# Kernel optimization log

Measured on AMD Instinct MI355X. Metric: run time of the kernel, lower is better.

## Reference

```python
import jax, jax.numpy as jnp
import numpy as np
import math

H = 8        # num_heads
D = 32       # dim_head
DEPTH = 1
LAMBDA_INIT = 0.8 - 0.6 * math.exp(-0.3 * DEPTH)
EPS = 1e-8


def setup_inputs() -> dict:
    key = jax.random.key(0)
    ks = jax.random.split(key, 9)
    B, T, IN_DIM, OUT_DIM = 2, 2048, 1024, 1024
    E = 2 * H * D  # 512
    inp = {
        "x": jax.random.normal(ks[0], (B, T, IN_DIM), dtype=jnp.float32),
        "Wq": jax.random.normal(ks[1], (IN_DIM, E), dtype=jnp.float32) * (IN_DIM ** -0.5),
        "Wkv": jax.random.normal(ks[2], (IN_DIM, 2 * E), dtype=jnp.float32) * (IN_DIM ** -0.5),
        "Wout": jax.random.normal(ks[3], (E, OUT_DIM), dtype=jnp.float32) * (E ** -0.5),
        "lambda_q1": 0.1 * jax.random.normal(ks[4], (D,), dtype=jnp.float32),
        "lambda_k1": 0.1 * jax.random.normal(ks[5], (D,), dtype=jnp.float32),
        "lambda_q2": 0.1 * jax.random.normal(ks[6], (D,), dtype=jnp.float32),
        "lambda_k2": 0.1 * jax.random.normal(ks[7], (D,), dtype=jnp.float32),
        "gamma": jnp.ones((2 * D,), dtype=jnp.float32),
    }
    return inp


def reference(x, Wq, Wkv, Wout, lambda_q1, lambda_k1, lambda_q2, lambda_k2, gamma):
    B, T, _ = x.shape
    scaling = D ** -0.5

    q = (x @ Wq).reshape(B, T, 2 * H, D).transpose(0, 2, 1, 3) * scaling  # [B,2H,T,D]
    kv = x @ Wkv
    k, v = jnp.split(kv, 2, axis=-1)
    k = k.reshape(B, T, 2 * H, D).transpose(0, 2, 1, 3)        # [B,2H,T,D]
    v = v.reshape(B, T, H, 2 * D).transpose(0, 2, 1, 3)        # [B,H,T,2D]

    dots = jnp.einsum('bhqd,bhkd->bhqk', q, k)                 # [B,2H,T,T]
    attn_w = jax.nn.softmax(dots.astype(jnp.float32), axis=-1).astype(dots.dtype)

    lam1 = jnp.exp(jnp.sum(lambda_q1 * lambda_k1))
    lam2 = jnp.exp(jnp.sum(lambda_q2 * lambda_k2))
    lam = lam1 - lam2 + LAMBDA_INIT

    attn_w = attn_w.reshape(B, H, 2, T, T)
    attn_w = attn_w[:, :, 0] - lam * attn_w[:, :, 1]           # [B,H,T,T]

    attn = jnp.einsum('bhqk,bhkd->bhqd', attn_w, v)            # [B,H,T,2D]

    rms = jnp.sqrt(jnp.mean(attn * attn, axis=-1, keepdims=True))
    attn = gamma * (attn / (rms + EPS))
    attn = attn * (1.0 - LAMBDA_INIT)

    attn = attn.transpose(0, 2, 1, 3).reshape(B, T, 2 * H * D)  # [B,T,E]
    return attn @ Wout
```

## Files before the change

kernel.cpp:

```cpp
#include <hip/hip_runtime.h>

typedef __attribute__((ext_vector_type(8)))  _Float16 half8;
typedef __attribute__((ext_vector_type(4)))  _Float16 half4;
typedef __attribute__((ext_vector_type(2)))  __fp16   fp16x2;
typedef __attribute__((ext_vector_type(4)))  float    f32x4;

#define MFMA16(a,b,c) __builtin_amdgcn_mfma_f32_16x16x32_f16(a,b,c,0,0,0)

#define QSCALE       0.17677669529663687f
#define LAMBDA_INIT  0.3555090675909693f
#define OUT_SCALE    0.6444909324090307f
#define LOG2E        1.4426950408889634f
#define MSHIFT       4.0f

#define EXP2(x) __builtin_amdgcn_exp2f(x)

__device__ __forceinline__ void gld16(const void* g, void* l) {
    __builtin_amdgcn_global_load_lds(
        (const __attribute__((address_space(1))) unsigned int*)g,
        (__attribute__((address_space(3))) unsigned int*)l, 16, 0, 0);
}

__device__ __forceinline__ void tr64(const float* __restrict__ src,
                                     _Float16* __restrict__ dst,
                                     int srcld, int dstld, int bx, int by) {
    __shared__ float t[64][65];
    int k0 = bx * 64, n0 = by * 64;
    int c = threadIdx.x & 63, rr = threadIdx.x >> 6;
#pragma unroll
    for (int ph = 0; ph < 16; ++ph) {
        int k = ph * 4 + rr;
        t[k][c] = src[(size_t)(k0 + k) * srcld + n0 + c];
    }
    __syncthreads();
#pragma unroll
    for (int ph = 0; ph < 16; ++ph) {
        int n = ph * 4 + rr;
        dst[(size_t)(n0 + n) * dstld + k0 + c] = (_Float16)t[c][n];
    }
}

__global__ __launch_bounds__(256) void k_prep(const float* __restrict__ x,
                                              const float* __restrict__ Wq,
                                              const float* __restrict__ Wkv,
                                              const float* __restrict__ Wout,
                                              _Float16* __restrict__ xh,
                                              _Float16* __restrict__ WallT,
                                              _Float16* __restrict__ WoutT) {
    int b = blockIdx.x;
    if (b < 4096) {
        int i = (b * 256 + threadIdx.x) * 4;
        f32x4 v = *(const f32x4*)(x + i);
        half4 h;
        h[0] = (_Float16)v[0]; h[1] = (_Float16)v[1];
        h[2] = (_Float16)v[2]; h[3] = (_Float16)v[3];
        *(half4*)(xh + i) = h;
    } else if (b < 4224) {
        int idx = b - 4096;
        tr64(Wq, WallT, 512, 1024, idx & 15, idx >> 4);
    } else if (b < 4480) {
        int idx = b - 4224;
        tr64(Wkv, WallT + 512 * 1024, 1024, 1024, idx & 15, idx >> 4);
    } else {
        int idx = b - 4480;
        tr64(Wout, WoutT, 1024, 512, idx & 7, idx >> 3);
    }
}

__device__ __forceinline__ void gemm_loop(const _Float16* __restrict__ A,
                                          const _Float16* __restrict__ Bt,
                                          int K, int bm, int bn,
                                          char* As, char* Bs,
                                          f32x4 (&acc)[4][4]) {
    int tid = threadIdx.x, lane = tid & 63, w = tid >> 6;
    int col16 = lane & 15, quad = lane >> 4;
    int wm = (w >> 1) << 6, wn = (w & 1) << 6;
    int r0 = tid >> 2;
    int kc = (tid & 3) << 3;
    const _Float16* ga0 = A  + (size_t)(bm + r0) * K + kc;
    const _Float16* ga1 = A  + (size_t)(bm + 64 + r0) * K + kc;
    const _Float16* gb0 = Bt + (size_t)(bn + r0) * K + kc;
    const _Float16* gb1 = Bt + (size_t)(bn + 64 + r0) * K + kc;
    char* lA = As + (w << 10);
    char* lB = Bs + (w << 10);

    for (int k0 = 0; k0 < K; k0 += 32) {
        __syncthreads();
        gld16(ga0 + k0, lA);
        gld16(ga1 + k0, lA + 4096);
        gld16(gb0 + k0, lB);
        gld16(gb1 + k0, lB + 4096);
        __syncthreads();
        half8 af[4], bf[4];
#pragma unroll
        for (int i = 0; i < 4; ++i)
            af[i] = *(const half8*)(As + ((wm + i * 16 + col16) << 6) + (quad << 4));
#pragma unroll
        for (int j = 0; j < 4; ++j)
            bf[j] = *(const half8*)(Bs + ((wn + j * 16 + col16) << 6) + (quad << 4));
#pragma unroll
        for (int i = 0; i < 4; ++i)
#pragma unroll
            for (int j = 0; j < 4; ++j)
                acc[i][j] = MFMA16(af[i], bf[j], acc[i][j]);
    }
}

__global__ __launch_bounds__(256) void k_gemm_qkv(const _Float16* __restrict__ xh,
                                                  const _Float16* __restrict__ WallT,
                                                  _Float16* __restrict__ qbuf,
                                                  char* __restrict__ Kf,
                                                  char* __restrict__ Vf) {
    __shared__ __align__(16) char As[8192];
    __shared__ __align__(16) char Bs[8192];
    f32x4 acc[4][4] = {};
    int bm = blockIdx.x * 128, bn = blockIdx.y * 128;
    gemm_loop(xh, WallT, 1024, bm, bn, As, Bs, acc);

    int tid = threadIdx.x, lane = tid & 63, w = tid >> 6;
    int col16 = lane & 15, quad = lane >> 4;
    int wm = (w >> 1) << 6, wn = (w & 1) << 6;

    if (bn < 512) {
        const float s = QSCALE * LOG2E;
#pragma unroll
        for (int i = 0; i < 4; ++i)
#pragma unroll
            for (int j = 0; j < 4; ++j) {
                int n = bn + wn + j * 16 + col16;
                int m0 = bm + wm + i * 16 + quad * 4;
#pragma unroll
                for (int r = 0; r < 4; ++r)
                    qbuf[(size_t)(m0 + r) * 512 + n] = (_Float16)(acc[i][j][r] * s);
            }
    } else if (bn < 1024) {
#pragma unroll
        for (int j = 0; j < 4; ++j) {
            int n = bn + wn + j * 16 + col16 - 512;
            int pp = n >> 6, dd = n & 63, head = dd >> 5, d32 = dd & 31;
            int lbase = (d32 >> 3) << 4;
            int e2 = (d32 & 7) << 1;
            int fragb = head << 11;
#pragma unroll
            for (int i = 0; i < 4; ++i) {
                int m0 = bm + wm + i * 16 + quad * 4;
                int b = m0 >> 11, tok = m0 & 2047, kb = tok >> 5, kk = tok & 31;
                char* dst = Kf + (((size_t)((b * 8 + pp) * 64 + kb)) << 12)
                          + fragb + ((kk >> 4) << 10) + ((lbase + (kk & 15)) << 4) + e2;
#pragma unroll
                for (int r = 0; r < 4; ++r)
                    *(_Float16*)(dst + (r << 4)) = (_Float16)acc[i][j][r];
            }
        }
    } else {
#pragma unroll
        for (int j = 0; j < 4; ++j) {
            int n = bn + wn + j * 16 + col16 - 1024;
            int pp = n >> 6, ch = n & 63;
            int off_t = ((ch >> 4) << 10) + ((ch & 15) << 4);
#pragma unroll
            for (int i = 0; i < 4; ++i) {
                int m0 = bm + wm + i * 16 + quad * 4;
                int b = m0 >> 11, tok = m0 & 2047, kb = tok >> 5, kk = tok & 31;
                int quadv = (kk < 16) ? (kk >> 2) : ((kk - 16) >> 2);
                int e0 = (kk < 16) ? 0 : 4;
                half4 hv;
#pragma unroll
                for (int r = 0; r < 4; ++r) hv[r] = (_Float16)acc[i][j][r];
                *(half4*)(Vf + (((size_t)((b * 8 + pp) * 64 + kb)) << 12)
                          + off_t + (quadv << 8) + (e0 << 1)) = hv;
            }
        }
    }
}

__global__ __launch_bounds__(256) void k_attn(const _Float16* __restrict__ qbuf,
                                              const char* __restrict__ Kf,
                                              const char* __restrict__ Vf,
                                              _Float16* __restrict__ Po0,
                                              _Float16* __restrict__ Po1,
                                              float* __restrict__ Pl,
                                              int nc) {
    __shared__ __align__(16) char Sh[32768];

    int blk = blockIdx.x;
    int qt = blk & 31, p = (blk >> 5) & 7, bb = (blk >> 8) & 1, c = blk >> 9;
    int tid = threadIdx.x, lane = tid & 63, w = tid >> 6;
    int col16 = lane & 15, quad = lane >> 4;
    int iters = 32 / nc;

    int qrow = bb * 2048 + qt * 64 + w * 16 + col16;
    const _Float16* qb = qbuf + (size_t)qrow * 512 + p * 64;
    half8 q1 = *(const half8*)(qb + quad * 8);
    half8 q2 = *(const half8*)(qb + 32 + quad * 8);

    size_t choff = (size_t)c * ((size_t)iters << 13);
    const char* Kb = Kf + (((size_t)(bb * 8 + p)) << 18) + choff;
    const char* Vb = Vf + (((size_t)(bb * 8 + p)) << 18) + choff;
    const f32x4 minit = {-MSHIFT, -MSHIFT, -MSHIFT, -MSHIFT};
    int t16 = tid << 4;

    float l1 = 0.f, l2 = 0.f;
    f32x4 o1[4] = {}, o2[4] = {};
    {
        gld16(Kb + t16, Sh + t16);          gld16(Kb + 4096 + t16, Sh + 4096 + t16);
        gld16(Vb + t16, Sh + 8192 + t16);   gld16(Vb + 4096 + t16, Sh + 12288 + t16);
    }
    for (int it = 0; it < iters; ++it) {
        __syncthreads();
        const char* cur = Sh + ((it & 1) << 14);
        if (it + 1 < iters) {
            const char* sk = Kb + ((size_t)(it + 1) << 13);
            const char* sv = Vb + ((size_t)(it + 1) << 13);
            char* d = Sh + (((it + 1) & 1) << 14);
            gld16(sk + t16, d + t16);          gld16(sk + 4096 + t16, d + 4096 + t16);
            gld16(sv + t16, d + 8192 + t16);   gld16(sv + 4096 + t16, d + 12288 + t16);
        }
#pragma unroll
        for (int g = 0; g < 2; ++g) {
            const char* kbase = cur + (g << 12) + (lane << 4);
            const char* vbase = cur + 8192 + (g << 12) + (lane << 4);
            half8 kf0 = *(const half8*)(kbase);
            half8 kf1 = *(const half8*)(kbase + 1024);
            half8 kf2 = *(const half8*)(kbase + 2048);
            half8 kf3 = *(const half8*)(kbase + 3072);
            f32x4 sa1 = MFMA16(kf0, q1, minit), sb1 = MFMA16(kf1, q1, minit);
            f32x4 sa2 = MFMA16(kf2, q2, minit), sb2 = MFMA16(kf3, q2, minit);

            union { half8 v; fp16x2 h[4]; } p1u, p2u;
            {
                float a0 = EXP2(sa1[0]), a1 = EXP2(sa1[1]);
                float a2 = EXP2(sa1[2]), a3 = EXP2(sa1[3]);
                float b0 = EXP2(sb1[0]), b1 = EXP2(sb1[1]);
                float b2 = EXP2(sb1[2]), b3 = EXP2(sb1[3]);
                l1 += ((a0 + a1) + (a2 + a3)) + ((b0 + b1) + (b2 + b3));
                p1u.h[0] = __builtin_amdgcn_cvt_pkrtz(a0, a1);
                p1u.h[1] = __builtin_amdgcn_cvt_pkrtz(a2, a3);
                p1u.h[2] = __builtin_amdgcn_cvt_pkrtz(b0, b1);
                p1u.h[3] = __builtin_amdgcn_cvt_pkrtz(b2, b3);
            }
            {
                float a0 = EXP2(sa2[0]), a1 = EXP2(sa2[1]);
                float a2 = EXP2(sa2[2]), a3 = EXP2(sa2[3]);
                float b0 = EXP2(sb2[0]), b1 = EXP2(sb2[1]);
                float b2 = EXP2(sb2[2]), b3 = EXP2(sb2[3]);
                l2 += ((a0 + a1) + (a2 + a3)) + ((b0 + b1) + (b2 + b3));
                p2u.h[0] = __builtin_amdgcn_cvt_pkrtz(a0, a1);
                p2u.h[1] = __builtin_amdgcn_cvt_pkrtz(a2, a3);
                p2u.h[2] = __builtin_amdgcn_cvt_pkrtz(b0, b1);
                p2u.h[3] = __builtin_amdgcn_cvt_pkrtz(b2, b3);
            }
            half8 vf0 = *(const half8*)(vbase);
            half8 vf1 = *(const half8*)(vbase + 1024);
            half8 vf2 = *(const half8*)(vbase + 2048);
            half8 vf3 = *(const half8*)(vbase + 3072);
            o1[0] = MFMA16(p1u.v, vf0, o1[0]); o2[0] = MFMA16(p2u.v, vf0, o2[0]);
            o1[1] = MFMA16(p1u.v, vf1, o1[1]); o2[1] = MFMA16(p2u.v, vf1, o2[1]);
            o1[2] = MFMA16(p1u.v, vf2, o1[2]); o2[2] = MFMA16(p2u.v, vf2, o2[2]);
            o1[3] = MFMA16(p1u.v, vf3, o1[3]); o2[3] = MFMA16(p2u.v, vf3, o2[3]);
        }
    }
    l1 += __shfl_xor(l1, 16); l1 += __shfl_xor(l1, 32);
    l2 += __shfl_xor(l2, 16); l2 += __shfl_xor(l2, 32);

    _Float16* Po = (c == 0) ? Po0 : Po1;
    int rowbase = (bb * 8 + p) * 2048 + qt * 64 + w * 16;
    _Float16* PoC = Po + (size_t)rowbase * 128;
#pragma unroll
    for (int r = 0; r < 4; ++r) {
        int rl = quad * 4 + r;
        _Float16* dst = PoC + (size_t)rl * 128 + col16;
#pragma unroll
        for (int t = 0; t < 4; ++t) {
            dst[t * 16]      = (_Float16)o1[t][r];
            dst[64 + t * 16] = (_Float16)o2[t][r];
        }
    }
    if (quad == 0) {
        int idx = rowbase + col16;
        Pl[c * 65536 + idx]         = l1;
        Pl[c * 65536 + 32768 + idx] = l2;
    }
}

__global__ __launch_bounds__(256) void k_combine(const _Float16* __restrict__ Po0,
                                                 const _Float16* __restrict__ Po1,
                                                 const float* __restrict__ Pl,
                                                 const float* __restrict__ lq1,
                                                 const float* __restrict__ lk1,
                                                 const float* __restrict__ lq2,
                                                 const float* __restrict__ lk2,
                                                 const float* __restrict__ gamma,
                                                 _Float16* __restrict__ attnO,
                                                 int nc) {
    int gid = blockIdx.x * 256 + threadIdx.x;
    int idx = gid >> 4, j = gid & 15;

    float s1 = 0.f, s2 = 0.f;
#pragma unroll
    for (int i = 0; i < 32; ++i) { s1 += lq1[i] * lk1[i]; s2 += lq2[i] * lk2[i]; }
    float lam = __expf(s1) - __expf(s2) + LAMBDA_INIT;

    size_t rb = (size_t)idx * 128 + j * 4;
    half4 c1a = *(const half4*)(Po0 + rb);
    half4 c2a = *(const half4*)(Po0 + rb + 64);
    float l1 = Pl[idx], l2 = Pl[32768 + idx];
    float o1[4], o2[4];
#pragma unroll
    for (int e = 0; e < 4; ++e) { o1[e] = (float)c1a[e]; o2[e] = (float)c2a[e]; }
    if (nc == 2) {
        half4 c1b = *(const half4*)(Po1 + rb);
        half4 c2b = *(const half4*)(Po1 + rb + 64);
        l1 += Pl[65536 + idx]; l2 += Pl[65536 + 32768 + idx];
#pragma unroll
        for (int e = 0; e < 4; ++e) { o1[e] += (float)c1b[e]; o2[e] += (float)c2b[e]; }
    }
    float il1 = 1.f / l1, il2 = lam / l2;
    float Of[4], ss = 0.f;
#pragma unroll
    for (int e = 0; e < 4; ++e) {
        Of[e] = o1[e] * il1 - o2[e] * il2;
        ss += Of[e] * Of[e];
    }
    ss += __shfl_xor(ss, 1, 16); ss += __shfl_xor(ss, 2, 16);
    ss += __shfl_xor(ss, 4, 16); ss += __shfl_xor(ss, 8, 16);
    float rms = sqrtf(ss * 0.015625f);
    float sc = OUT_SCALE / (rms + 1e-8f);

    int b = idx >> 14, p = (idx >> 11) & 7, t = idx & 2047;
    half4 o;
#pragma unroll
    for (int e = 0; e < 4; ++e) o[e] = (_Float16)(gamma[j * 4 + e] * Of[e] * sc);
    *(half4*)(attnO + ((size_t)(b * 2048 + t) * 512) + p * 64 + j * 4) = o;
}

__global__ __launch_bounds__(256) void k_gemm_out(const _Float16* __restrict__ attn,
                                                  const _Float16* __restrict__ WoutT,
                                                  float* __restrict__ out) {
    __shared__ __align__(16) char As[8192];
    __shared__ __align__(16) char Bs[8192];
    f32x4 acc[4][4] = {};
    int bm = blockIdx.x * 128, bn = blockIdx.y * 128;
    gemm_loop(attn, WoutT, 512, bm, bn, As, Bs, acc);

    int tid = threadIdx.x, lane = tid & 63, w = tid >> 6;
    int col16 = lane & 15, quad = lane >> 4;
    int wm = (w >> 1) << 6, wn = (w & 1) << 6;
#pragma unroll
    for (int i = 0; i < 4; ++i)
#pragma unroll
        for (int j = 0; j < 4; ++j) {
            int n = bn + wn + j * 16 + col16;
            int m0 = bm + wm + i * 16 + quad * 4;
#pragma unroll
            for (int r = 0; r < 4; ++r)
                out[(size_t)(m0 + r) * 1024 + n] = acc[i][j][r];
        }
}

extern "C" void kernel_launch(void* const* d_in, const int* in_sizes, int n_in,
                              void* d_out, int out_size, void* d_ws, size_t ws_size,
                              hipStream_t stream) {
    const float* x     = (const float*)d_in[0];
    const float* Wq    = (const float*)d_in[1];
    const float* Wkv   = (const float*)d_in[2];
    const float* Wout  = (const float*)d_in[3];
    const float* lq1   = (const float*)d_in[4];
    const float* lk1   = (const float*)d_in[5];
    const float* lq2   = (const float*)d_in[6];
    const float* lk2   = (const float*)d_in[7];
    const float* gamma = (const float*)d_in[8];
    float* out = (float*)d_out;

    char* ws = (char*)d_ws;
    _Float16* xh    = (_Float16*)(ws);
    _Float16* Po0   = (_Float16*)(ws);
    _Float16* WallT = (_Float16*)(ws + 8388608);
    float*    Pl    = (float*)(ws + 8388608);
    _Float16* WoutT = (_Float16*)(ws + 11534336);
    _Float16* qbuf  = (_Float16*)(ws + 12582912);
    char*     Kf    = (char*)(ws + 16777216);
    char*     Vf    = (char*)(ws + 20971520);
    _Float16* attn  = (_Float16*)(ws + 25165824);
    _Float16* Po1   = (_Float16*)(ws + 29360128);

    int nc = (ws_size >= 37748736u) ? 2 : 1;

    k_prep<<<4608, 256, 0, stream>>>(x, Wq, Wkv, Wout, xh, WallT, WoutT);
    k_gemm_qkv<<<dim3(32, 12), 256, 0, stream>>>(xh, WallT, qbuf, Kf, Vf);
    k_attn<<<nc * 512, 256, 0, stream>>>(qbuf, Kf, Vf, Po0, Po1, Pl, nc);
    k_combine<<<2048, 256, 0, stream>>>(Po0, Po1, Pl, lq1, lk1, lq2, lk2, gamma, attn, nc);
    k_gemm_out<<<dim3(32, 8), 256, 0, stream>>>(attn, WoutT, out);
}
```

Before: 169.0 us.

## Fuse attention split-K combine into attention kernel with in-block chunk reduction

Replaces the separate attention and combine kernels with one kernel of 512-thread blocks, where 4 wave pairs each cover a quarter of the key range for 32 query rows. Partial outputs and row sums are reduced through shared memory, and the lambda-difference, RMS norm and output store happen in the same block. This removes the global round trip of fp16 partials and one launch. The new loop drops double buffering and uses two barriers per iteration, so load latency is no longer overlapped with compute.

```diff
diff --git a/kernel.cpp b/kernel.cpp
--- a/kernel.cpp
+++ b/kernel.cpp
@@ -174,164 +174,137 @@
     }
 }
 
-__global__ __launch_bounds__(256) void k_attn(const _Float16* __restrict__ qbuf,
-                                              const char* __restrict__ Kf,
-                                              const char* __restrict__ Vf,
-                                              _Float16* __restrict__ Po0,
-                                              _Float16* __restrict__ Po1,
-                                              float* __restrict__ Pl,
-                                              int nc) {
+__global__ __launch_bounds__(512, 8) void k_attn_fused(
+        const _Float16* __restrict__ qbuf,
+        const char* __restrict__ Kf,
+        const char* __restrict__ Vf,
+        const float* __restrict__ lq1,
+        const float* __restrict__ lk1,
+        const float* __restrict__ lq2,
+        const float* __restrict__ lk2,
+        const float* __restrict__ gamma,
+        _Float16* __restrict__ attnO) {
     __shared__ __align__(16) char Sh[32768];
+    __shared__ float Ls[2][8][16];
 
     int blk = blockIdx.x;
-    int qt = blk & 31, p = (blk >> 5) & 7, bb = (blk >> 8) & 1, c = blk >> 9;
+    int r32 = blk & 63, p = (blk >> 6) & 7, bb = blk >> 9;
     int tid = threadIdx.x, lane = tid & 63, w = tid >> 6;
+    int qt2 = w & 1, c = w >> 1;
     int col16 = lane & 15, quad = lane >> 4;
-    int iters = 32 / nc;
-
-    int qrow = bb * 2048 + qt * 64 + w * 16 + col16;
+
+    int qrow = bb * 2048 + r32 * 32 + qt2 * 16 + col16;
     const _Float16* qb = qbuf + (size_t)qrow * 512 + p * 64;
     half8 q1 = *(const half8*)(qb + quad * 8);
     half8 q2 = *(const half8*)(qb + 32 + quad * 8);
 
-    size_t choff = (size_t)c * ((size_t)iters << 13);
-    const char* Kb = Kf + (((size_t)(bb * 8 + p)) << 18) + choff;
-    const char* Vb = Vf + (((size_t)(bb * 8 + p)) << 18) + choff;
+    size_t bpoff = ((size_t)(bb * 8 + p)) << 18;
+    const char* src2 = ((tid >= 256) ? Vf : Kf) + bpoff + ((tid & 255) << 4);
+    int dbase = ((tid >= 256) ? 4096 : 0) + ((tid & 255) << 4);
+
+    const char* kvb = Sh + (c << 13) + (lane << 4);
     const f32x4 minit = {-MSHIFT, -MSHIFT, -MSHIFT, -MSHIFT};
-    int t16 = tid << 4;
 
     float l1 = 0.f, l2 = 0.f;
     f32x4 o1[4] = {}, o2[4] = {};
-    {
-        gld16(Kb + t16, Sh + t16);          gld16(Kb + 4096 + t16, Sh + 4096 + t16);
-        gld16(Vb + t16, Sh + 8192 + t16);   gld16(Vb + 4096 + t16, Sh + 12288 + t16);
-    }
-    for (int it = 0; it < iters; ++it) {
+
+    for (int it = 0; it < 16; ++it) {
         __syncthreads();
-        const char* cur = Sh + ((it & 1) << 14);
-        if (it + 1 < iters) {
-            const char* sk = Kb + ((size_t)(it + 1) << 13);
-            const char* sv = Vb + ((size_t)(it + 1) << 13);
-            char* d = Sh + (((it + 1) & 1) << 14);
-            gld16(sk + t16, d + t16);          gld16(sk + 4096 + t16, d + 4096 + t16);
-            gld16(sv + t16, d + 8192 + t16);   gld16(sv + 4096 + t16, d + 12288 + t16);
-        }
-#pragma unroll
-        for (int g = 0; g < 2; ++g) {
-            const char* kbase = cur + (g << 12) + (lane << 4);
-            const char* vbase = cur + 8192 + (g << 12) + (lane << 4);
-            half8 kf0 = *(const half8*)(kbase);
-            half8 kf1 = *(const half8*)(kbase + 1024);
-            half8 kf2 = *(const half8*)(kbase + 2048);
-            half8 kf3 = *(const half8*)(kbase + 3072);
-            f32x4 sa1 = MFMA16(kf0, q1, minit), sb1 = MFMA16(kf1, q1, minit);
-            f32x4 sa2 = MFMA16(kf2, q2, minit), sb2 = MFMA16(kf3, q2, minit);
-
-            union { half8 v; fp16x2 h[4]; } p1u, p2u;
-            {
-                float a0 = EXP2(sa1[0]), a1 = EXP2(sa1[1]);
-                float a2 = EXP2(sa1[2]), a3 = EXP2(sa1[3]);
-                float b0 = EXP2(sb1[0]), b1 = EXP2(sb1[1]);
-                float b2 = EXP2(sb1[2]), b3 = EXP2(sb1[3]);
-                l1 += ((a0 + a1) + (a2 + a3)) + ((b0 + b1) + (b2 + b3));
-                p1u.h[0] = __builtin_amdgcn_cvt_pkrtz(a0, a1);
-                p1u.h[1] = __builtin_amdgcn_cvt_pkrtz(a2, a3);
-                p1u.h[2] = __builtin_amdgcn_cvt_pkrtz(b0, b1);
-                p1u.h[3] = __builtin_amdgcn_cvt_pkrtz(b2, b3);
-            }
-            {
-                float a0 = EXP2(sa2[0]), a1 = EXP2(sa2[1]);
-                float a2 = EXP2(sa2[2]), a3 = EXP2(sa2[3]);
-                float b0 = EXP2(sb2[0]), b1 = EXP2(sb2[1]);
-                float b2 = EXP2(sb2[2]), b3 = EXP2(sb2[3]);
-                l2 += ((a0 + a1) + (a2 + a3)) + ((b0 + b1) + (b2 + b3));
-                p2u.h[0] = __builtin_amdgcn_cvt_pkrtz(a0, a1);
-                p2u.h[1] = __builtin_amdgcn_cvt_pkrtz(a2, a3);
-                p2u.h[2] = __builtin_amdgcn_cvt_pkrtz(b0, b1);
-                p2u.h[3] = __builtin_amdgcn_cvt_pkrtz(b2, b3);
-            }
-            half8 vf0 = *(const half8*)(vbase);
-            half8 vf1 = *(const half8*)(vbase + 1024);
-            half8 vf2 = *(const half8*)(vbase + 2048);
-            half8 vf3 = *(const half8*)(vbase + 3072);
-            o1[0] = MFMA16(p1u.v, vf0, o1[0]); o2[0] = MFMA16(p2u.v, vf0, o2[0]);
-            o1[1] = MFMA16(p1u.v, vf1, o1[1]); o2[1] = MFMA16(p2u.v, vf1, o2[1]);
-            o1[2] = MFMA16(p1u.v, vf2, o1[2]); o2[2] = MFMA16(p2u.v, vf2, o2[2]);
-            o1[3] = MFMA16(p1u.v, vf3, o1[3]); o2[3] = MFMA16(p2u.v, vf3, o2[3]);
-        }
-    }
+#pragma unroll
+        for (int j = 0; j < 4; ++j)
+            gld16(src2 + ((size_t)((j << 4) + it) << 12), (char*)Sh + (j << 13) + dbase);
+        __syncthreads();
+
+        half8 kf0 = *(const half8*)(kvb);
+        half8 kf1 = *(const half8*)(kvb + 1024);
+        half8 kf2 = *(const half8*)(kvb + 2048);
+        half8 kf3 = *(const half8*)(kvb + 3072);
+        f32x4 sa1 = MFMA16(kf0, q1, minit), sb1 = MFMA16(kf1, q1, minit);
+        f32x4 sa2 = MFMA16(kf2, q2, minit), sb2 = MFMA16(kf3, q2, minit);
+
+        union { half8 v; fp16x2 h[4]; } p1u, p2u;
+        {
+            float a0 = EXP2(sa1[0]), a1 = EXP2(sa1[1]);
+            float a2 = EXP2(sa1[2]), a3 = EXP2(sa1[3]);
+            float b0 = EXP2(sb1[0]), b1 = EXP2(sb1[1]);
+            float b2 = EXP2(sb1[2]), b3 = EXP2(sb1[3]);
+            l1 += ((a0 + a1) + (a2 + a3)) + ((b0 + b1) + (b2 + b3));
+            p1u.h[0] = __builtin_amdgcn_cvt_pkrtz(a0, a1);
+            p1u.h[1] = __builtin_amdgcn_cvt_pkrtz(a2, a3);
+            p1u.h[2] = __builtin_amdgcn_cvt_pkrtz(b0, b1);
+            p1u.h[3] = __builtin_amdgcn_cvt_pkrtz(b2, b3);
+        }
+        {
+            float a0 = EXP2(sa2[0]), a1 = EXP2(sa2[1]);
+            float a2 = EXP2(sa2[2]), a3 = EXP2(sa2[3]);
+            float b0 = EXP2(sb2[0]), b1 = EXP2(sb2[1]);
+            float b2 = EXP2(sb2[2]), b3 = EXP2(sb2[3]);
+            l2 += ((a0 + a1) + (a2 + a3)) + ((b0 + b1) + (b2 + b3));
+            p2u.h[0] = __builtin_amdgcn_cvt_pkrtz(a0, a1);
+            p2u.h[1] = __builtin_amdgcn_cvt_pkrtz(a2, a3);
+            p2u.h[2] = __builtin_amdgcn_cvt_pkrtz(b0, b1);
+            p2u.h[3] = __builtin_amdgcn_cvt_pkrtz(b2, b3);
+        }
+        half8 vf0 = *(const half8*)(kvb + 4096);
+        half8 vf1 = *(const half8*)(kvb + 5120);
+        half8 vf2 = *(const half8*)(kvb + 6144);
+        half8 vf3 = *(const half8*)(kvb + 7168);
+        o1[0] = MFMA16(p1u.v, vf0, o1[0]); o2[0] = MFMA16(p2u.v, vf0, o2[0]);
+        o1[1] = MFMA16(p1u.v, vf1, o1[1]); o2[1] = MFMA16(p2u.v, vf1, o2[1]);
+        o1[2] = MFMA16(p1u.v, vf2, o1[2]); o2[2] = MFMA16(p2u.v, vf2, o2[2]);
+        o1[3] = MFMA16(p1u.v, vf3, o1[3]); o2[3] = MFMA16(p2u.v, vf3, o2[3]);
+    }
+
     l1 += __shfl_xor(l1, 16); l1 += __shfl_xor(l1, 32);
     l2 += __shfl_xor(l2, 16); l2 += __shfl_xor(l2, 32);
 
-    _Float16* Po = (c == 0) ? Po0 : Po1;
-    int rowbase = (bb * 8 + p) * 2048 + qt * 64 + w * 16;
-    _Float16* PoC = Po + (size_t)rowbase * 128;
-#pragma unroll
-    for (int r = 0; r < 4; ++r) {
-        int rl = quad * 4 + r;
-        _Float16* dst = PoC + (size_t)rl * 128 + col16;
-#pragma unroll
-        for (int t = 0; t < 4; ++t) {
-            dst[t * 16]      = (_Float16)o1[t][r];
-            dst[64 + t * 16] = (_Float16)o2[t][r];
-        }
-    }
-    if (quad == 0) {
-        int idx = rowbase + col16;
-        Pl[c * 65536 + idx]         = l1;
-        Pl[c * 65536 + 32768 + idx] = l2;
-    }
-}
-
-__global__ __launch_bounds__(256) void k_combine(const _Float16* __restrict__ Po0,
-                                                 const _Float16* __restrict__ Po1,
-                                                 const float* __restrict__ Pl,
-                                                 const float* __restrict__ lq1,
-                                                 const float* __restrict__ lk1,
-                                                 const float* __restrict__ lq2,
-                                                 const float* __restrict__ lk2,
-                                                 const float* __restrict__ gamma,
-                                                 _Float16* __restrict__ attnO,
-                                                 int nc) {
-    int gid = blockIdx.x * 256 + threadIdx.x;
-    int idx = gid >> 4, j = gid & 15;
-
+    __syncthreads();
+    {
+        _Float16* ob = (_Float16*)(Sh + ((c * 2 + qt2) << 12)) + col16;
+#pragma unroll
+        for (int r = 0; r < 4; ++r) {
+            _Float16* od = ob + (quad * 4 + r) * 128;
+#pragma unroll
+            for (int t = 0; t < 4; ++t) {
+                od[t * 16]      = (_Float16)o1[t][r];
+                od[64 + t * 16] = (_Float16)o2[t][r];
+            }
+        }
+        if (quad == 0) { Ls[0][w][col16] = l1; Ls[1][w][col16] = l2; }
+    }
+    __syncthreads();
+
+    int rr = tid >> 4, jj = tid & 15;
+    int qrt = rr >> 4, r16 = rr & 15;
+    float o1s[4] = {}, o2s[4] = {};
+    float l1s = 0.f, l2s = 0.f;
+#pragma unroll
+    for (int cc = 0; cc < 4; ++cc) {
+        const _Float16* ob = (const _Float16*)(Sh + ((cc * 2 + qrt) << 12))
+                           + r16 * 128 + jj * 4;
+        half4 a  = *(const half4*)ob;
+        half4 b2 = *(const half4*)(ob + 64);
+#pragma unroll
+        for (int e = 0; e < 4; ++e) { o1s[e] += (float)a[e]; o2s[e] += (float)b2[e]; }
+        l1s += Ls[0][cc * 2 + qrt][r16];
+        l2s += Ls[1][cc * 2 + qrt][r16];
+    }
     float s1 = 0.f, s2 = 0.f;
 #pragma unroll
     for (int i = 0; i < 32; ++i) { s1 += lq1[i] * lk1[i]; s2 += lq2[i] * lk2[i]; }
     float lam = __expf(s1) - __expf(s2) + LAMBDA_INIT;
-
-    size_t rb = (size_t)idx * 128 + j * 4;
-    half4 c1a = *(const half4*)(Po0 + rb);
-    half4 c2a = *(const half4*)(Po0 + rb + 64);
-    float l1 = Pl[idx], l2 = Pl[32768 + idx];
-    float o1[4], o2[4];
-#pragma unroll
-    for (int e = 0; e < 4; ++e) { o1[e] = (float)c1a[e]; o2[e] = (float)c2a[e]; }
-    if (nc == 2) {
-        half4 c1b = *(const half4*)(Po1 + rb);
-        half4 c2b = *(const half4*)(Po1 + rb + 64);
-        l1 += Pl[65536 + idx]; l2 += Pl[65536 + 32768 + idx];
-#pragma unroll
-        for (int e = 0; e < 4; ++e) { o1[e] += (float)c1b[e]; o2[e] += (float)c2b[e]; }
-    }
-    float il1 = 1.f / l1, il2 = lam / l2;
+    float il1 = 1.f / l1s, il2 = lam / l2s;
     float Of[4], ss = 0.f;
 #pragma unroll
-    for (int e = 0; e < 4; ++e) {
-        Of[e] = o1[e] * il1 - o2[e] * il2;
-        ss += Of[e] * Of[e];
-    }
+    for (int e = 0; e < 4; ++e) { Of[e] = o1s[e] * il1 - o2s[e] * il2; ss += Of[e] * Of[e]; }
     ss += __shfl_xor(ss, 1, 16); ss += __shfl_xor(ss, 2, 16);
     ss += __shfl_xor(ss, 4, 16); ss += __shfl_xor(ss, 8, 16);
     float rms = sqrtf(ss * 0.015625f);
     float sc = OUT_SCALE / (rms + 1e-8f);
-
-    int b = idx >> 14, p = (idx >> 11) & 7, t = idx & 2047;
     half4 o;
 #pragma unroll
-    for (int e = 0; e < 4; ++e) o[e] = (_Float16)(gamma[j * 4 + e] * Of[e] * sc);
-    *(half4*)(attnO + ((size_t)(b * 2048 + t) * 512) + p * 64 + j * 4) = o;
+    for (int e = 0; e < 4; ++e) o[e] = (_Float16)(gamma[jj * 4 + e] * Of[e] * sc);
+    *(half4*)(attnO + ((size_t)(bb * 2048 + r32 * 32 + rr) * 512) + p * 64 + jj * 4) = o;
 }
 
 __global__ __launch_bounds__(256) void k_gemm_out(const _Float16* __restrict__ attn,
@@ -374,21 +347,15 @@
 
     char* ws = (char*)d_ws;
     _Float16* xh    = (_Float16*)(ws);
-    _Float16* Po0   = (_Float16*)(ws);
     _Float16* WallT = (_Float16*)(ws + 8388608);
-    float*    Pl    = (float*)(ws + 8388608);
     _Float16* WoutT = (_Float16*)(ws + 11534336);
     _Float16* qbuf  = (_Float16*)(ws + 12582912);
     char*     Kf    = (char*)(ws + 16777216);
     char*     Vf    = (char*)(ws + 20971520);
     _Float16* attn  = (_Float16*)(ws + 25165824);
-    _Float16* Po1   = (_Float16*)(ws + 29360128);
-
-    int nc = (ws_size >= 37748736u) ? 2 : 1;
 
     k_prep<<<4608, 256, 0, stream>>>(x, Wq, Wkv, Wout, xh, WallT, WoutT);
     k_gemm_qkv<<<dim3(32, 12), 256, 0, stream>>>(xh, WallT, qbuf, Kf, Vf);
-    k_attn<<<nc * 512, 256, 0, stream>>>(qbuf, Kf, Vf, Po0, Po1, Pl, nc);
-    k_combine<<<2048, 256, 0, stream>>>(Po0, Po1, Pl, lq1, lk1, lq2, lk2, gamma, attn, nc);
+    k_attn_fused<<<1024, 512, 0, stream>>>(qbuf, Kf, Vf, lq1, lk1, lq2, lk2, gamma, attn);
     k_gemm_out<<<dim3(32, 8), 256, 0, stream>>>(attn, WoutT, out);
 }
```

After: 309.9 us. 83.4% more time.
